# Kernel optimization log

Measured on AMD Instinct MI355X. Metric: run time of the kernel, lower is better.

Reference implementation:

```python
import jax, jax.numpy as jnp
import numpy as np

K = 3  # kernel size per dim


def _conv3d(x, w, b):
    # x: (N,C,T,H,W), w: (O,C,3,3,3), stride 1, padding 1
    y = jax.lax.conv_general_dilated(
        x, w, window_strides=(1, 1, 1),
        padding=((1, 1), (1, 1), (1, 1)),
        dimension_numbers=('NCDHW', 'OIDHW', 'NCDHW'))
    return y + b[None, :, None, None, None]


def _dcn_hw(x, w_off, b_off, w, b):
    """DeformConvPack_d with dimension='HW': offsets only along H and W."""
    N, C, T, H, W = x.shape
    KK = K * K * K  # 27 taps
    # offset prediction conv: (N, 2*27, T, H, W) -> (N, 27, 2, T, H, W)
    off = _conv3d(x, w_off, b_off).reshape(N, KK, 2, T, H, W)
    kt, kh, kw = [a.reshape(-1) for a in jnp.meshgrid(
        jnp.arange(K), jnp.arange(K), jnp.arange(K), indexing='ij')]
    # temporal sampling positions are integer (no offset along T)
    p_t = jnp.arange(T)[None, :] + kt[:, None] - 1              # (27, T)
    t_ok = ((p_t >= 0) & (p_t < T))[None, :, :, None, None]     # (1,27,T,1,1)
    p_tc = jnp.clip(p_t, 0, T - 1)[None, :, :, None, None]
    # fractional spatial sampling positions: (N,27,T,H,W)
    p_h = (jnp.arange(H, dtype=x.dtype)[None, None, None, :, None]
           + (kh - 1).astype(x.dtype)[None, :, None, None, None] + off[:, :, 0])
    p_w = (jnp.arange(W, dtype=x.dtype)[None, None, None, None, :]
           + (kw - 1).astype(x.dtype)[None, :, None, None, None] + off[:, :, 1])
    h0f = jnp.floor(p_h); w0f = jnp.floor(p_w)
    lh = (p_h - h0f)[..., None]; lw = (p_w - w0f)[..., None]
    h0 = h0f.astype(jnp.int32); w0 = w0f.astype(jnp.int32)
    xt = jnp.transpose(x, (0, 2, 3, 4, 1))  # (N,T,H,W,C) for gather
    bidx = jnp.arange(N)[:, None, None, None, None]

    def corner(hi, wi):
        ok = t_ok & (hi >= 0) & (hi < H) & (wi >= 0) & (wi < W)
        v = xt[bidx, p_tc, jnp.clip(hi, 0, H - 1), jnp.clip(wi, 0, W - 1)]
        return jnp.where(ok[..., None], v, jnp.zeros((), x.dtype))

    # bilinear interpolation with zero padding outside bounds
    samp = ((1 - lh) * (1 - lw)) * corner(h0, w0) \
         + ((1 - lh) * lw) * corner(h0, w0 + 1) \
         + (lh * (1 - lw)) * corner(h0 + 1, w0) \
         + (lh * lw) * corner(h0 + 1, w0 + 1)     # (N,27,T,H,W,C)
    O = w.shape[0]
    out = jnp.einsum('nkthwc,ock->nothw', samp, w.reshape(O, C, KK))
    return out + b[None, :, None, None, None]


def setup_inputs() -> dict:
    key = jax.random.key(0)
    ks = jax.random.split(key, 6)
    N, C, T, H, W = 1, 64, 7, 48, 48
    fan = 1.0 / np.sqrt(C * 27)
    return {
        'x': jax.random.normal(ks[0], (N, C, T, H, W), jnp.float32),
        'w_off0': jax.random.normal(ks[1], (54, C, 3, 3, 3), jnp.float32) * 0.01,
        'b_off0': jnp.zeros((54,), jnp.float32),
        'w0': jax.random.normal(ks[2], (C, C, 3, 3, 3), jnp.float32) * fan,
        'b0': jnp.zeros((C,), jnp.float32),
        'w_off1': jax.random.normal(ks[3], (54, C, 3, 3, 3), jnp.float32) * 0.01,
        'b_off1': jnp.zeros((54,), jnp.float32),
        'w1': jax.random.normal(ks[4], (C, C, 3, 3, 3), jnp.float32) * fan,
        'b1': jnp.zeros((C,), jnp.float32),
    }


def reference(x, w_off0, b_off0, w0, b0, w_off1, b_off1, w1, b1):
    h = _dcn_hw(x, w_off0, b_off0, w0, b0)
    h = jnp.where(h >= 0, h, 0.1 * h)  # LeakyReLU(0.1)
    return _dcn_hw(h, w_off1, b_off1, w1, b1) + x
```

## Files before the change

### kernel.cpp

```cpp
#include <hip/hip_runtime.h>

#define T_ 7
#define H_ 48
#define W_ 48
#define P_ 16128
#define HW_ 2304

typedef __attribute__((ext_vector_type(8))) short short8;
typedef __attribute__((ext_vector_type(4))) float f32x4;
typedef __attribute__((ext_vector_type(4))) unsigned u32x4;

__device__ __forceinline__ unsigned short f2bf(float f) {
  union { float f; unsigned u; } x{f};
  unsigned r = x.u + 0x7FFFu + ((x.u >> 16) & 1u);
  return (unsigned short)(r >> 16);
}
__device__ __forceinline__ float blo(unsigned u) {
  union { unsigned u; float f; } x{u << 16};
  return x.f;
}
__device__ __forceinline__ float bhi(unsigned u) {
  union { unsigned u; float f; } x{u & 0xFFFF0000u};
  return x.f;
}
__device__ __forceinline__ unsigned pack2(float a, float b) {
  return (unsigned)f2bf(a) | ((unsigned)f2bf(b) << 16);
}
__device__ __forceinline__ int xcd_swz(int bid, int nwg) {
  int cpx = nwg >> 3;
  return (bid & 7) * cpx + (bid >> 3);
}

struct Wgt { short8 b00, b01, b10, b11, b20, b21, b30, b31; };

__device__ __forceinline__ Wgt load_w(const unsigned short* base, int k, int lane) {
  const unsigned short* wp = base + (size_t)k * 4096 + lane * 8;
  Wgt w;
  w.b00 = *(const short8*)(wp);
  w.b01 = *(const short8*)(wp + 512);
  w.b10 = *(const short8*)(wp + 1024);
  w.b11 = *(const short8*)(wp + 1536);
  w.b20 = *(const short8*)(wp + 2048);
  w.b21 = *(const short8*)(wp + 2560);
  w.b30 = *(const short8*)(wp + 3072);
  w.b31 = *(const short8*)(wp + 3584);
  return w;
}

__device__ __forceinline__ void mfma8(const Wgt& W, short8 af0, short8 af1,
                                      f32x4& c0, f32x4& c1, f32x4& c2, f32x4& c3) {
  c0 = __builtin_amdgcn_mfma_f32_16x16x32_bf16(af0, W.b00, c0, 0, 0, 0);
  c0 = __builtin_amdgcn_mfma_f32_16x16x32_bf16(af1, W.b01, c0, 0, 0, 0);
  c1 = __builtin_amdgcn_mfma_f32_16x16x32_bf16(af0, W.b10, c1, 0, 0, 0);
  c1 = __builtin_amdgcn_mfma_f32_16x16x32_bf16(af1, W.b11, c1, 0, 0, 0);
  c2 = __builtin_amdgcn_mfma_f32_16x16x32_bf16(af0, W.b20, c2, 0, 0, 0);
  c2 = __builtin_amdgcn_mfma_f32_16x16x32_bf16(af1, W.b21, c2, 0, 0, 0);
  c3 = __builtin_amdgcn_mfma_f32_16x16x32_bf16(af0, W.b30, c3, 0, 0, 0);
  c3 = __builtin_amdgcn_mfma_f32_16x16x32_bf16(af1, W.b31, c3, 0, 0, 0);
}

__global__ void k_prep_x(const float* __restrict__ in, unsigned short* __restrict__ outb) {
  __shared__ float tile[64][65];
  int p0 = blockIdx.x * 64;
  int l = threadIdx.x & 63;
  int g = threadIdx.x >> 6;
#pragma unroll
  for (int i = 0; i < 16; ++i) {
    int c = g * 16 + i;
    tile[c][l] = in[c * P_ + p0 + l];
  }
  __syncthreads();
#pragma unroll
  for (int i = 0; i < 16; ++i) {
    int p = g * 16 + i;
    outb[(p0 + p) * 64 + l] = f2bf(tile[l][p]);
  }
}

__global__ void k_prep_w4(const float* __restrict__ s0, const float* __restrict__ s1,
                          const float* __restrict__ s2, const float* __restrict__ s3,
                          unsigned short* __restrict__ d0, unsigned short* __restrict__ d1,
                          unsigned short* __restrict__ d2, unsigned short* __restrict__ d3) {
  int y = blockIdx.y;
  const float* w = (y == 0) ? s0 : (y == 1) ? s1 : (y == 2) ? s2 : s3;
  unsigned short* wt = (y == 0) ? d0 : (y == 1) ? d1 : (y == 2) ? d2 : d3;
  int OC = (y < 2) ? 54 : 64;
  int idx = blockIdx.x * 256 + threadIdx.x;
  int j = idx & 7;
  int l = (idx >> 3) & 63;
  int kc = (idx >> 9) & 1;
  int nt = (idx >> 10) & 3;
  int k = idx >> 12;
  int o = nt * 16 + (l & 15);
  int c = kc * 32 + (l >> 4) * 8 + j;
  wt[idx] = (o < OC) ? f2bf(w[(o * 64 + c) * 27 + k]) : (unsigned short)0;
}

__global__ __launch_bounds__(256) void k_off4w(const unsigned short* __restrict__ xclb,
                                               const unsigned short* __restrict__ wAs,
                                               const float* __restrict__ boff,
                                               float* __restrict__ offt2) {
  __shared__ f32x4 red[4][4][64];
  int p0 = xcd_swz(blockIdx.x, gridDim.x) * 32;
  int t = p0 / HW_;
  int r0 = p0 - t * HW_;
  int h0r = r0 / W_;
  int w0s = r0 - h0r * W_;
  int h1r = h0r + (w0s == 32 ? 1 : 0);
  int w1s = (w0s == 32) ? 0 : w0s + 16;
  int tid = threadIdx.x;
  int lane = tid & 63, wid = tid >> 6;
  int pt = lane & 15, grp = lane >> 4;

  f32x4 zacc{0.f, 0.f, 0.f, 0.f};
  f32x4 aA0 = zacc, aA1 = zacc, aA2 = zacc, aA3 = zacc;
  f32x4 aB0 = zacc, aB1 = zacc, aB2 = zacc, aB3 = zacc;
  const short8 zero8{0, 0, 0, 0, 0, 0, 0, 0};
  int kbeg = wid * 7;

#pragma unroll
  for (int kk = 0; kk < 7; ++kk) {
    int kraw = kbeg + kk;
    int k = min(kraw, 26);
    int kt = k / 9;
    int r9 = k - kt * 9;
    int kh = r9 / 3;
    int kw = r9 - (r9 / 3) * 3;
    int t2 = t + kt - 1;
    bool tok = (kraw < 27) & ((unsigned)t2 < (unsigned)T_);
    int t2c = min(max(t2, 0), T_ - 1);

    Wgt W = load_w(wAs, k, lane);
    {
      int h2 = h0r + kh - 1;
      int w2 = w0s + pt + kw - 1;
      bool ok = tok & ((unsigned)h2 < (unsigned)H_) & ((unsigned)w2 < (unsigned)W_);
      int h2c = min(max(h2, 0), H_ - 1);
      int w2c = min(max(w2, 0), W_ - 1);
      const unsigned short* ap = xclb + ((size_t)(t2c * HW_ + h2c * W_ + w2c) * 64 + grp * 8);
      short8 a0 = *(const short8*)ap;
      short8 a1 = *(const short8*)(ap + 32);
      a0 = ok ? a0 : zero8;
      a1 = ok ? a1 : zero8;
      mfma8(W, a0, a1, aA0, aA1, aA2, aA3);
    }
    {
      int h2 = h1r + kh - 1;
      int w2 = w1s + pt + kw - 1;
      bool ok = tok & ((unsigned)h2 < (unsigned)H_) & ((unsigned)w2 < (unsigned)W_);
      int h2c = min(max(h2, 0), H_ - 1);
      int w2c = min(max(w2, 0), W_ - 1);
      const unsigned short* ap = xclb + ((size_t)(t2c * HW_ + h2c * W_ + w2c) * 64 + grp * 8);
      short8 a0 = *(const short8*)ap;
      short8 a1 = *(const short8*)(ap + 32);
      a0 = ok ? a0 : zero8;
      a1 = ok ? a1 : zero8;
      mfma8(W, a0, a1, aB0, aB1, aB2, aB3);
    }
  }

  int oc = wid * 16 + pt;
  float bb = (oc < 54) ? boff[oc] : 0.f;
  int kidx = oc >> 1, d = oc & 1;

  red[wid][0][lane] = aA0;
  red[wid][1][lane] = aA1;
  red[wid][2][lane] = aA2;
  red[wid][3][lane] = aA3;
  __syncthreads();
  {
    f32x4 s = red[0][wid][lane];
    s = s + red[1][wid][lane];
    s = s + red[2][wid][lane];
    s = s + red[3][wid][lane];
    if (oc < 54) {
#pragma unroll
      for (int r = 0; r < 4; ++r) {
        int p = p0 + grp * 4 + r;
        offt2[((size_t)kidx * P_ + p) * 2 + d] = s[r] + bb;
      }
    }
  }
  __syncthreads();
  red[wid][0][lane] = aB0;
  red[wid][1][lane] = aB1;
  red[wid][2][lane] = aB2;
  red[wid][3][lane] = aB3;
  __syncthreads();
  {
    f32x4 s = red[0][wid][lane];
    s = s + red[1][wid][lane];
    s = s + red[2][wid][lane];
    s = s + red[3][wid][lane];
    if (oc < 54) {
#pragma unroll
      for (int r = 0; r < 4; ++r) {
        int p = p0 + 16 + grp * 4 + r;
        offt2[((size_t)kidx * P_ + p) * 2 + d] = s[r] + bb;
      }
    }
  }
}

template <int MODE>
__global__ __launch_bounds__(256) void k_samp_sc(
    const unsigned short* __restrict__ xclb, const float* __restrict__ offt2,
    const unsigned short* __restrict__ wBs, const float* __restrict__ bias,
    const float* __restrict__ resid, float* __restrict__ out32,
    unsigned short* __restrict__ outb) {
  __shared__ f32x4 red[4][4][64];
  __shared__ unsigned short sA[4][2][16][72];
  __shared__ u32x4 raw[4][16][2][16];
  __shared__ int abuf[4][16][2];
  int p0 = xcd_swz(blockIdx.x, gridDim.x) * 32;
  int t = p0 / HW_;
  int r0 = p0 - t * HW_;
  int h0r = r0 / W_;
  int w0s = r0 - h0r * W_;
  int h1r = h0r + (w0s == 32 ? 1 : 0);
  int w1s = (w0s == 32) ? 0 : w0s + 16;
  int tid = threadIdx.x;
  int lane = tid & 63, wid = tid >> 6;
  int pt = lane & 15, grp = lane >> 4;
  int lq = lane >> 4;
  int ck16 = lane & 15;

  f32x4 zacc{0.f, 0.f, 0.f, 0.f};
  f32x4 aA0 = zacc, aA1 = zacc, aA2 = zacc, aA3 = zacc;
  f32x4 aB0 = zacc, aB1 = zacc, aB2 = zacc, aB3 = zacc;
  int kbeg = wid * 7;

#pragma clang loop unroll(disable)
  for (int kk = 0; kk < 7; ++kk) {
    int kraw = kbeg + kk;
    int k = min(kraw, 26);
    int kt = k / 9;
    int r9 = k - kt * 9;
    int kh = r9 / 3;
    int kw = r9 - (r9 / 3) * 3;
    int t2 = t + kt - 1;
    bool tok = (kraw < 27) & ((unsigned)t2 < (unsigned)T_);
    int t2c = min(max(t2, 0), T_ - 1);

    Wgt W = load_w(wBs, k, lane);

#pragma unroll
    for (int f = 0; f < 2; ++f) {
      int hrow = f ? h1r : h0r;
      int wst = f ? w1s : w0s;
      float2 o2 = *(const float2*)(offt2 + ((size_t)k * P_ + p0 + f * 16 + pt) * 2);
      float ph = (float)(hrow + kh - 1) + o2.x;
      float pw = (float)(wst + pt + kw - 1) + o2.y;
      float hf = floorf(ph), wf = floorf(pw);
      float lh = ph - hf, lw = pw - wf;
      int h0 = (int)hf, w0i = (int)wf;
      int h1 = h0 + 1, w1 = w0i + 1;
      bool h0ok = ((unsigned)h0 < (unsigned)H_), h1ok = ((unsigned)h1 < (unsigned)H_);
      bool w0ok = ((unsigned)w0i < (unsigned)W_), w1ok = ((unsigned)w1 < (unsigned)W_);
      int h0c = min(max(h0, 0), H_ - 1), h1c = min(max(h1, 0), H_ - 1);
      int w0c = min(max(w0i, 0), W_ - 1), w1c = min(max(w1, 0), W_ - 1);
      float omlh = 1.f - lh, omlw = 1.f - lw;
      float g00 = (tok & h0ok & w0ok) ? omlh * omlw : 0.f;
      float g01 = (tok & h0ok & w1ok) ? omlh * lw : 0.f;
      float g10 = (tok & h1ok & w0ok) ? lh * omlw : 0.f;
      float g11 = (tok & h1ok & w1ok) ? lh * lw : 0.f;

      int ws = min(max(w0i, 0), W_ - 2);
      int sel0 = w0c - ws;
      int sel1 = w1c - ws;
      if (grp == 0) {
        abuf[wid][pt][0] = (t2c * HW_ + h0c * W_ + ws) * 64;
        abuf[wid][pt][1] = (t2c * HW_ + h1c * W_ + ws) * 64;
      }
      __builtin_amdgcn_wave_barrier();

      u32x4 gb0, gb1, gb2, gb3, gb4, gb5, gb6, gb7;
      {
        int pl0 = lq, pl1 = 4 + lq, pl2 = 8 + lq, pl3 = 12 + lq;
        const unsigned short* c0p = xclb + (size_t)abuf[wid][pl0][0] + ck16 * 8;
        const unsigned short* c1p = xclb + (size_t)abuf[wid][pl0][1] + ck16 * 8;
        const unsigned short* c2p = xclb + (size_t)abuf[wid][pl1][0] + ck16 * 8;
        const unsigned short* c3p = xclb + (size_t)abuf[wid][pl1][1] + ck16 * 8;
        const unsigned short* c4p = xclb + (size_t)abuf[wid][pl2][0] + ck16 * 8;
        const unsigned short* c5p = xclb + (size_t)abuf[wid][pl2][1] + ck16 * 8;
        const unsigned short* c6p = xclb + (size_t)abuf[wid][pl3][0] + ck16 * 8;
        const unsigned short* c7p = xclb + (size_t)abuf[wid][pl3][1] + ck16 * 8;
        gb0 = *(const u32x4*)c0p;
        gb1 = *(const u32x4*)c1p;
        gb2 = *(const u32x4*)c2p;
        gb3 = *(const u32x4*)c3p;
        gb4 = *(const u32x4*)c4p;
        gb5 = *(const u32x4*)c5p;
        gb6 = *(const u32x4*)c6p;
        gb7 = *(const u32x4*)c7p;
      }
      __builtin_amdgcn_wave_barrier();
      {
        int pl0 = lq, pl1 = 4 + lq, pl2 = 8 + lq, pl3 = 12 + lq;
        raw[wid][pl0][0][ck16 ^ pl0] = gb0;
        raw[wid][pl0][1][ck16 ^ pl0] = gb1;
        raw[wid][pl1][0][ck16 ^ pl1] = gb2;
        raw[wid][pl1][1][ck16 ^ pl1] = gb3;
        raw[wid][pl2][0][ck16 ^ pl2] = gb4;
        raw[wid][pl2][1][ck16 ^ pl2] = gb5;
        raw[wid][pl3][0][ck16 ^ pl3] = gb6;
        raw[wid][pl3][1][ck16 ^ pl3] = gb7;
      }
      __builtin_amdgcn_wave_barrier();

      int b0 = sel0 * 8 + 2 * grp;
      int b1 = sel1 * 8 + 2 * grp;
      u32x4 A0 = raw[wid][pt][0][(b0) ^ pt];
      u32x4 A1 = raw[wid][pt][0][(b0 + 1) ^ pt];
      u32x4 B0 = raw[wid][pt][0][(b1) ^ pt];
      u32x4 B1 = raw[wid][pt][0][(b1 + 1) ^ pt];
      u32x4 C0 = raw[wid][pt][1][(b0) ^ pt];
      u32x4 C1 = raw[wid][pt][1][(b0 + 1) ^ pt];
      u32x4 D0 = raw[wid][pt][1][(b1) ^ pt];
      u32x4 D1 = raw[wid][pt][1][(b1 + 1) ^ pt];
      __builtin_amdgcn_wave_barrier();

#define LERPU(a, b, c, d)                                                   \
  pack2(g00 * blo(a) + g01 * blo(b) + g10 * blo(c) + g11 * blo(d),          \
        g00 * bhi(a) + g01 * bhi(b) + g10 * bhi(c) + g11 * bhi(d))
      u32x4 v0, v1;
      v0[0] = LERPU(A0[0], B0[0], C0[0], D0[0]);
      v0[1] = LERPU(A0[1], B0[1], C0[1], D0[1]);
      v0[2] = LERPU(A0[2], B0[2], C0[2], D0[2]);
      v0[3] = LERPU(A0[3], B0[3], C0[3], D0[3]);
      v1[0] = LERPU(A1[0], B1[0], C1[0], D1[0]);
      v1[1] = LERPU(A1[1], B1[1], C1[1], D1[1]);
      v1[2] = LERPU(A1[2], B1[2], C1[2], D1[2]);
      v1[3] = LERPU(A1[3], B1[3], C1[3], D1[3]);
#undef LERPU

      __builtin_amdgcn_wave_barrier();
      *(u32x4*)&sA[wid][f][pt][grp * 16] = v0;
      *(u32x4*)&sA[wid][f][pt][grp * 16 + 8] = v1;
      __builtin_amdgcn_wave_barrier();
      short8 af0 = *(const short8*)&sA[wid][f][pt][grp * 8];
      short8 af1 = *(const short8*)&sA[wid][f][pt][32 + grp * 8];
      __builtin_amdgcn_wave_barrier();

      if (f == 0) mfma8(W, af0, af1, aA0, aA1, aA2, aA3);
      else        mfma8(W, af0, af1, aB0, aB1, aB2, aB3);
    }
  }

  int ch = wid * 16 + pt;
  float bb = bias[ch];

  red[wid][0][lane] = aA0;
  red[wid][1][lane] = aA1;
  red[wid][2][lane] = aA2;
  red[wid][3][lane] = aA3;
  __syncthreads();
  {
    f32x4 s = red[0][wid][lane];
    s = s + red[1][wid][lane];
    s = s + red[2][wid][lane];
    s = s + red[3][wid][lane];
#pragma unroll
    for (int r = 0; r < 4; ++r) {
      int p = p0 + grp * 4 + r;
      float v = s[r] + bb;
      if (MODE == 0) {
        v = (v >= 0.f) ? v : 0.1f * v;
        outb[(size_t)p * 64 + ch] = f2bf(v);
      } else {
        out32[(size_t)ch * P_ + p] = v + resid[(size_t)ch * P_ + p];
      }
    }
  }
  __syncthreads();
  red[wid][0][lane] = aB0;
  red[wid][1][lane] = aB1;
  red[wid][2][lane] = aB2;
  red[wid][3][lane] = aB3;
  __syncthreads();
  {
    f32x4 s = red[0][wid][lane];
    s = s + red[1][wid][lane];
    s = s + red[2][wid][lane];
    s = s + red[3][wid][lane];
#pragma unroll
    for (int r = 0; r < 4; ++r) {
      int p = p0 + 16 + grp * 4 + r;
      float v = s[r] + bb;
      if (MODE == 0) {
        v = (v >= 0.f) ? v : 0.1f * v;
        outb[(size_t)p * 64 + ch] = f2bf(v);
      } else {
        out32[(size_t)ch * P_ + p] = v + resid[(size_t)ch * P_ + p];
      }
    }
  }
}

extern "C" void kernel_launch(void* const* d_in, const int* in_sizes, int n_in,
                              void* d_out, int out_size, void* d_ws, size_t ws_size,
                              hipStream_t stream) {
  const float* x      = (const float*)d_in[0];
  const float* w_off0 = (const float*)d_in[1];
  const float* b_off0 = (const float*)d_in[2];
  const float* w0     = (const float*)d_in[3];
  const float* b0     = (const float*)d_in[4];
  const float* w_off1 = (const float*)d_in[5];
  const float* b_off1 = (const float*)d_in[6];
  const float* w1     = (const float*)d_in[7];
  const float* b1     = (const float*)d_in[8];
  float* out = (float*)d_out;

  char* base = (char*)d_ws;
  unsigned short* x_clb = (unsigned short*)base;
  unsigned short* h_clb = (unsigned short*)(base + 2064384);
  float*          offt2 = (float*)(base + 4128768);
  unsigned short* wA0   = (unsigned short*)(base + 7612416);
  unsigned short* wA1   = (unsigned short*)(base + 7833600);
  unsigned short* wB0   = (unsigned short*)(base + 8054784);
  unsigned short* wB1   = (unsigned short*)(base + 8275968);

  hipLaunchKernelGGL(k_prep_x, dim3(252), dim3(256), 0, stream, x, x_clb);
  hipLaunchKernelGGL(k_prep_w4, dim3(432, 4), dim3(256), 0, stream,
                     w_off0, w_off1, w0, w1, wA0, wA1, wB0, wB1);

  hipLaunchKernelGGL(k_off4w, dim3(504), dim3(256), 0, stream, x_clb, wA0, b_off0, offt2);
  hipLaunchKernelGGL((k_samp_sc<0>), dim3(504), dim3(256), 0, stream,
                     x_clb, offt2, wB0, b0, (const float*)nullptr, (float*)nullptr, h_clb);

  hipLaunchKernelGGL(k_off4w, dim3(504), dim3(256), 0, stream, h_clb, wA1, b_off1, offt2);
  hipLaunchKernelGGL((k_samp_sc<1>), dim3(504), dim3(256), 0, stream,
                     h_clb, offt2, wB1, b1, x, out, (unsigned short*)nullptr);
}
```

Measured before the change: 86.58 us.

## Split fused deformable sampling+GEMM into separate sample-generation and GEMM kernels

Replaces the fused sampling/MFMA kernel with two kernels. The first builds a bf16 im2col-style buffer of bilinearly sampled values for all 27 taps, using cross-lane shuffles in place of LDS staging. The second streams that buffer into MFMA with a fully unrolled tap loop. This removes per-wave LDS round-trips and wave barriers from the GEMM path. In exchange it writes and re-reads a ~55 MB intermediate per layer and adds two extra launches.

```diff
diff --git a/kernel.cpp b/kernel.cpp
--- a/kernel.cpp
+++ b/kernel.cpp
@@ -202,153 +202,127 @@
   }
 }
 
-template <int MODE>
-__global__ __launch_bounds__(256) void k_samp_sc(
-    const unsigned short* __restrict__ xclb, const float* __restrict__ offt2,
-    const unsigned short* __restrict__ wBs, const float* __restrict__ bias,
-    const float* __restrict__ resid, float* __restrict__ out32,
-    unsigned short* __restrict__ outb) {
-  __shared__ f32x4 red[4][4][64];
-  __shared__ unsigned short sA[4][2][16][72];
-  __shared__ u32x4 raw[4][16][2][16];
-  __shared__ int abuf[4][16][2];
-  int p0 = xcd_swz(blockIdx.x, gridDim.x) * 32;
+__global__ __launch_bounds__(256) void k_sampgen(
+    const unsigned short* __restrict__ src, const float* __restrict__ offt2,
+    unsigned short* __restrict__ samp) {
+  int p0 = xcd_swz(blockIdx.x, gridDim.x) * 16;
   int t = p0 / HW_;
-  int r0 = p0 - t * HW_;
-  int h0r = r0 / W_;
-  int w0s = r0 - h0r * W_;
-  int h1r = h0r + (w0s == 32 ? 1 : 0);
-  int w1s = (w0s == 32) ? 0 : w0s + 16;
-  int tid = threadIdx.x;
-  int lane = tid & 63, wid = tid >> 6;
-  int pt = lane & 15, grp = lane >> 4;
-  int lq = lane >> 4;
-  int ck16 = lane & 15;
-
-  f32x4 zacc{0.f, 0.f, 0.f, 0.f};
-  f32x4 aA0 = zacc, aA1 = zacc, aA2 = zacc, aA3 = zacc;
-  f32x4 aB0 = zacc, aB1 = zacc, aB2 = zacc, aB3 = zacc;
-  int kbeg = wid * 7;
-
-#pragma clang loop unroll(disable)
-  for (int kk = 0; kk < 7; ++kk) {
-    int kraw = kbeg + kk;
-    int k = min(kraw, 26);
+  int lane = threadIdx.x & 63, wid = threadIdx.x >> 6;
+  int q = lane >> 4;
+  int sub = lane & 15;
+  int v = sub >> 3;
+  int chr = sub & 7;
+  int p = p0 + wid * 4 + q;
+  int rr = p - t * HW_;
+  int h_p = rr / W_;
+  int w_p = rr - h_p * W_;
+
+  for (int k = 0; k < 27; ++k) {
     int kt = k / 9;
     int r9 = k - kt * 9;
     int kh = r9 / 3;
     int kw = r9 - (r9 / 3) * 3;
     int t2 = t + kt - 1;
-    bool tok = (kraw < 27) & ((unsigned)t2 < (unsigned)T_);
+    bool tok = (unsigned)t2 < (unsigned)T_;
     int t2c = min(max(t2, 0), T_ - 1);
 
+    float2 o2 = *(const float2*)(offt2 + ((size_t)k * P_ + p) * 2);
+    float ph = (float)(h_p + kh - 1) + o2.x;
+    float pw = (float)(w_p + kw - 1) + o2.y;
+    float hf = floorf(ph), wf = floorf(pw);
+    float lh = ph - hf, lw = pw - wf;
+    int h0 = (int)hf, w0i = (int)wf;
+    int h1 = h0 + 1, w1 = w0i + 1;
+    bool h0ok = ((unsigned)h0 < (unsigned)H_), h1ok = ((unsigned)h1 < (unsigned)H_);
+    bool w0ok = ((unsigned)w0i < (unsigned)W_), w1ok = ((unsigned)w1 < (unsigned)W_);
+    int h0c = min(max(h0, 0), H_ - 1), h1c = min(max(h1, 0), H_ - 1);
+    int w0c = min(max(w0i, 0), W_ - 1), w1c = min(max(w1, 0), W_ - 1);
+    float omlh = 1.f - lh, omlw = 1.f - lw;
+    float g00 = (tok & h0ok & w0ok) ? omlh * omlw : 0.f;
+    float g01 = (tok & h0ok & w1ok) ? omlh * lw : 0.f;
+    float g10 = (tok & h1ok & w0ok) ? lh * omlw : 0.f;
+    float g11 = (tok & h1ok & w1ok) ? lh * lw : 0.f;
+
+    int ws = min(max(w0i, 0), W_ - 2);
+    int sel0 = w0c - ws;
+    int sel1 = w1c - ws;
+    const unsigned short* s0p = src + (size_t)(t2c * HW_ + h0c * W_ + ws) * 64 + sub * 8;
+    const unsigned short* s1p = src + (size_t)(t2c * HW_ + h1c * W_ + ws) * 64 + sub * 8;
+    u32x4 e0 = *(const u32x4*)s0p;
+    u32x4 e1 = *(const u32x4*)s1p;
+
+    u32x4 f0, f1;
+#pragma unroll
+    for (int j = 0; j < 4; ++j) {
+      f0[j] = (unsigned)__shfl_xor((int)e0[j], 8);
+      f1[j] = (unsigned)__shfl_xor((int)e1[j], 8);
+    }
+    u32x4 wA0v = (v == 0) ? e0 : f0;
+    u32x4 wB0v = (v == 0) ? f0 : e0;
+    u32x4 wA1v = (v == 0) ? e1 : f1;
+    u32x4 wB1v = (v == 0) ? f1 : e1;
+    u32x4 a = sel0 ? wB0v : wA0v;
+    u32x4 b = sel1 ? wB0v : wA0v;
+    u32x4 c = sel0 ? wB1v : wA1v;
+    u32x4 d = sel1 ? wB1v : wA1v;
+
+    u32x4 r;
+#pragma unroll
+    for (int j = 0; j < 4; ++j) {
+      float lo = g00 * blo(a[j]) + g01 * blo(b[j]) + g10 * blo(c[j]) + g11 * blo(d[j]);
+      float hi = g00 * bhi(a[j]) + g01 * bhi(b[j]) + g10 * bhi(c[j]) + g11 * bhi(d[j]);
+      r[j] = pack2(lo, hi);
+    }
+    if (v == 0) {
+      *(u32x4*)(samp + ((size_t)k * P_ + p) * 64 + chr * 8) = r;
+    }
+  }
+}
+
+template <int MODE>
+__global__ __launch_bounds__(256) void k_gemm(
+    const unsigned short* __restrict__ samp, const unsigned short* __restrict__ wBs,
+    const float* __restrict__ bias, const float* __restrict__ resid,
+    float* __restrict__ out32, unsigned short* __restrict__ outb) {
+  __shared__ f32x4 red[4][4][64];
+  int p0 = xcd_swz(blockIdx.x, gridDim.x) * 32;
+  int tid = threadIdx.x;
+  int lane = tid & 63, wid = tid >> 6;
+  int pt = lane & 15, grp = lane >> 4;
+
+  f32x4 zacc{0.f, 0.f, 0.f, 0.f};
+  f32x4 aA0 = zacc, aA1 = zacc, aA2 = zacc, aA3 = zacc;
+  f32x4 aB0 = zacc, aB1 = zacc, aB2 = zacc, aB3 = zacc;
+  const short8 zero8{0, 0, 0, 0, 0, 0, 0, 0};
+  int kbeg = wid * 7;
+
+#pragma unroll
+  for (int kk = 0; kk < 7; ++kk) {
+    int kraw = kbeg + kk;
+    int k = min(kraw, 26);
+    bool ok = (kraw < 27);
+
     Wgt W = load_w(wBs, k, lane);
-
-#pragma unroll
-    for (int f = 0; f < 2; ++f) {
-      int hrow = f ? h1r : h0r;
-      int wst = f ? w1s : w0s;
-      float2 o2 = *(const float2*)(offt2 + ((size_t)k * P_ + p0 + f * 16 + pt) * 2);
-      float ph = (float)(hrow + kh - 1) + o2.x;
-      float pw = (float)(wst + pt + kw - 1) + o2.y;
-      float hf = floorf(ph), wf = floorf(pw);
-      float lh = ph - hf, lw = pw - wf;
-      int h0 = (int)hf, w0i = (int)wf;
-      int h1 = h0 + 1, w1 = w0i + 1;
-      bool h0ok = ((unsigned)h0 < (unsigned)H_), h1ok = ((unsigned)h1 < (unsigned)H_);
-      bool w0ok = ((unsigned)w0i < (unsigned)W_), w1ok = ((unsigned)w1 < (unsigned)W_);
-      int h0c = min(max(h0, 0), H_ - 1), h1c = min(max(h1, 0), H_ - 1);
-      int w0c = min(max(w0i, 0), W_ - 1), w1c = min(max(w1, 0), W_ - 1);
-      float omlh = 1.f - lh, omlw = 1.f - lw;
-      float g00 = (tok & h0ok & w0ok) ? omlh * omlw : 0.f;
-      float g01 = (tok & h0ok & w1ok) ? omlh * lw : 0.f;
-      float g10 = (tok & h1ok & w0ok) ? lh * omlw : 0.f;
-      float g11 = (tok & h1ok & w1ok) ? lh * lw : 0.f;
-
-      int ws = min(max(w0i, 0), W_ - 2);
-      int sel0 = w0c - ws;
-      int sel1 = w1c - ws;
-      if (grp == 0) {
-        abuf[wid][pt][0] = (t2c * HW_ + h0c * W_ + ws) * 64;
-        abuf[wid][pt][1] = (t2c * HW_ + h1c * W_ + ws) * 64;
-      }
-      __builtin_amdgcn_wave_barrier();
-
-      u32x4 gb0, gb1, gb2, gb3, gb4, gb5, gb6, gb7;
-      {
-        int pl0 = lq, pl1 = 4 + lq, pl2 = 8 + lq, pl3 = 12 + lq;
-        const unsigned short* c0p = xclb + (size_t)abuf[wid][pl0][0] + ck16 * 8;
-        const unsigned short* c1p = xclb + (size_t)abuf[wid][pl0][1] + ck16 * 8;
-        const unsigned short* c2p = xclb + (size_t)abuf[wid][pl1][0] + ck16 * 8;
-        const unsigned short* c3p = xclb + (size_t)abuf[wid][pl1][1] + ck16 * 8;
-        const unsigned short* c4p = xclb + (size_t)abuf[wid][pl2][0] + ck16 * 8;
-        const unsigned short* c5p = xclb + (size_t)abuf[wid][pl2][1] + ck16 * 8;
-        const unsigned short* c6p = xclb + (size_t)abuf[wid][pl3][0] + ck16 * 8;
-        const unsigned short* c7p = xclb + (size_t)abuf[wid][pl3][1] + ck16 * 8;
-        gb0 = *(const u32x4*)c0p;
-        gb1 = *(const u32x4*)c1p;
-        gb2 = *(const u32x4*)c2p;
-        gb3 = *(const u32x4*)c3p;
-        gb4 = *(const u32x4*)c4p;
-        gb5 = *(const u32x4*)c5p;
-        gb6 = *(const u32x4*)c6p;
-        gb7 = *(const u32x4*)c7p;
-      }
-      __builtin_amdgcn_wave_barrier();
-      {
-        int pl0 = lq, pl1 = 4 + lq, pl2 = 8 + lq, pl3 = 12 + lq;
-        raw[wid][pl0][0][ck16 ^ pl0] = gb0;
-        raw[wid][pl0][1][ck16 ^ pl0] = gb1;
-        raw[wid][pl1][0][ck16 ^ pl1] = gb2;
-        raw[wid][pl1][1][ck16 ^ pl1] = gb3;
-        raw[wid][pl2][0][ck16 ^ pl2] = gb4;
-        raw[wid][pl2][1][ck16 ^ pl2] = gb5;
-        raw[wid][pl3][0][ck16 ^ pl3] = gb6;
-        raw[wid][pl3][1][ck16 ^ pl3] = gb7;
-      }
-      __builtin_amdgcn_wave_barrier();
-
-      int b0 = sel0 * 8 + 2 * grp;
-      int b1 = sel1 * 8 + 2 * grp;
-      u32x4 A0 = raw[wid][pt][0][(b0) ^ pt];
-      u32x4 A1 = raw[wid][pt][0][(b0 + 1) ^ pt];
-      u32x4 B0 = raw[wid][pt][0][(b1) ^ pt];
-      u32x4 B1 = raw[wid][pt][0][(b1 + 1) ^ pt];
-      u32x4 C0 = raw[wid][pt][1][(b0) ^ pt];
-      u32x4 C1 = raw[wid][pt][1][(b0 + 1) ^ pt];
-      u32x4 D0 = raw[wid][pt][1][(b1) ^ pt];
-      u32x4 D1 = raw[wid][pt][1][(b1 + 1) ^ pt];
-      __builtin_amdgcn_wave_barrier();
-
-#define LERPU(a, b, c, d)                                                   \
-  pack2(g00 * blo(a) + g01 * blo(b) + g10 * blo(c) + g11 * blo(d),          \
-        g00 * bhi(a) + g01 * bhi(b) + g10 * bhi(c) + g11 * bhi(d))
-      u32x4 v0, v1;
-      v0[0] = LERPU(A0[0], B0[0], C0[0], D0[0]);
-      v0[1] = LERPU(A0[1], B0[1], C0[1], D0[1]);
-      v0[2] = LERPU(A0[2], B0[2], C0[2], D0[2]);
-      v0[3] = LERPU(A0[3], B0[3], C0[3], D0[3]);
-      v1[0] = LERPU(A1[0], B1[0], C1[0], D1[0]);
-      v1[1] = LERPU(A1[1], B1[1], C1[1], D1[1]);
-      v1[2] = LERPU(A1[2], B1[2], C1[2], D1[2]);
-      v1[3] = LERPU(A1[3], B1[3], C1[3], D1[3]);
-#undef LERPU
-
-      __builtin_amdgcn_wave_barrier();
-      *(u32x4*)&sA[wid][f][pt][grp * 16] = v0;
-      *(u32x4*)&sA[wid][f][pt][grp * 16 + 8] = v1;
-      __builtin_amdgcn_wave_barrier();
-      short8 af0 = *(const short8*)&sA[wid][f][pt][grp * 8];
-      short8 af1 = *(const short8*)&sA[wid][f][pt][32 + grp * 8];
-      __builtin_amdgcn_wave_barrier();
-
-      if (f == 0) mfma8(W, af0, af1, aA0, aA1, aA2, aA3);
-      else        mfma8(W, af0, af1, aB0, aB1, aB2, aB3);
-    }
-  }
-
-  int ch = wid * 16 + pt;
-  float bb = bias[ch];
+    {
+      const unsigned short* ap = samp + ((size_t)k * P_ + p0 + pt) * 64 + grp * 8;
+      short8 a0 = *(const short8*)ap;
+      short8 a1 = *(const short8*)(ap + 32);
+      a0 = ok ? a0 : zero8;
+      a1 = ok ? a1 : zero8;
+      mfma8(W, a0, a1, aA0, aA1, aA2, aA3);
+    }
+    {
+      const unsigned short* ap = samp + ((size_t)k * P_ + p0 + 16 + pt) * 64 + grp * 8;
+      short8 a0 = *(const short8*)ap;
+      short8 a1 = *(const short8*)(ap + 32);
+      a0 = ok ? a0 : zero8;
+      a1 = ok ? a1 : zero8;
+      mfma8(W, a0, a1, aB0, aB1, aB2, aB3);
+    }
+  }
+
+  int oc = wid * 16 + pt;
+  float bb = bias[oc];
 
   red[wid][0][lane] = aA0;
   red[wid][1][lane] = aA1;
@@ -363,12 +337,12 @@
 #pragma unroll
     for (int r = 0; r < 4; ++r) {
       int p = p0 + grp * 4 + r;
-      float v = s[r] + bb;
+      float vv = s[r] + bb;
       if (MODE == 0) {
-        v = (v >= 0.f) ? v : 0.1f * v;
-        outb[(size_t)p * 64 + ch] = f2bf(v);
+        vv = (vv >= 0.f) ? vv : 0.1f * vv;
+        outb[(size_t)p * 64 + oc] = f2bf(vv);
       } else {
-        out32[(size_t)ch * P_ + p] = v + resid[(size_t)ch * P_ + p];
+        out32[(size_t)oc * P_ + p] = vv + resid[(size_t)oc * P_ + p];
       }
     }
   }
@@ -386,12 +360,12 @@
 #pragma unroll
     for (int r = 0; r < 4; ++r) {
       int p = p0 + 16 + grp * 4 + r;
-      float v = s[r] + bb;
+      float vv = s[r] + bb;
       if (MODE == 0) {
-        v = (v >= 0.f) ? v : 0.1f * v;
-        outb[(size_t)p * 64 + ch] = f2bf(v);
+        vv = (vv >= 0.f) ? vv : 0.1f * vv;
+        outb[(size_t)p * 64 + oc] = f2bf(vv);
       } else {
-        out32[(size_t)ch * P_ + p] = v + resid[(size_t)ch * P_ + p];
+        out32[(size_t)oc * P_ + p] = vv + resid[(size_t)oc * P_ + p];
       }
     }
   }
@@ -419,16 +393,19 @@
   unsigned short* wA1   = (unsigned short*)(base + 7833600);
   unsigned short* wB0   = (unsigned short*)(base + 8054784);
   unsigned short* wB1   = (unsigned short*)(base + 8275968);
+  unsigned short* samp  = (unsigned short*)(base + 8497152);
 
   hipLaunchKernelGGL(k_prep_x, dim3(252), dim3(256), 0, stream, x, x_clb);
   hipLaunchKernelGGL(k_prep_w4, dim3(432, 4), dim3(256), 0, stream,
                      w_off0, w_off1, w0, w1, wA0, wA1, wB0, wB1);
 
   hipLaunchKernelGGL(k_off4w, dim3(504), dim3(256), 0, stream, x_clb, wA0, b_off0, offt2);
-  hipLaunchKernelGGL((k_samp_sc<0>), dim3(504), dim3(256), 0, stream,
-                     x_clb, offt2, wB0, b0, (const float*)nullptr, (float*)nullptr, h_clb);
+  hipLaunchKernelGGL(k_sampgen, dim3(1008), dim3(256), 0, stream, x_clb, offt2, samp);
+  hipLaunchKernelGGL((k_gemm<0>), dim3(504), dim3(256), 0, stream,
+                     samp, wB0, b0, (const float*)nullptr, (float*)nullptr, h_clb);
 
   hipLaunchKernelGGL(k_off4w, dim3(504), dim3(256), 0, stream, h_clb, wA1, b_off1, offt2);
-  hipLaunchKernelGGL((k_samp_sc<1>), dim3(504), dim3(256), 0, stream,
-                     h_clb, offt2, wB1, b1, x, out, (unsigned short*)nullptr);
-}
+  hipLaunchKernelGGL(k_sampgen, dim3(1008), dim3(256), 0, stream, h_clb, offt2, samp);
+  hipLaunchKernelGGL((k_gemm<1>), dim3(504), dim3(256), 0, stream,
+                     samp, wB1, b1, x, out, (unsigned short*)nullptr);
+}
```

After: 141.6 us. 1.64x slower.
